# Performance work log

Hardware: AMD Instinct MI355X
Metric: run time of the kernel (lower is better)

The kernel has to match this reference:

```python
import jax, jax.numpy as jnp
import numpy as np

K = 20            # neighbors
C = 21            # num_classes
P = 16            # patch_size
NROWS = 14        # img_size // patch_size
H = NROWS * P     # 224
TEMP = 1.0        # temperature


def setup_inputs() -> dict:
    key = jax.random.key(0)
    k1, k2, k3 = jax.random.split(key, 3)
    test_feature = jax.random.normal(k1, (8, 196, 384), dtype=jnp.float32)
    train_features = jax.random.normal(k2, (384, 50000), dtype=jnp.float32)
    train_labels = jax.random.randint(k3, (256, 50000), 0, C, dtype=jnp.int32)
    return {"test_feature": test_feature, "train_features": train_features,
            "train_labels": train_labels}


def reference(test_feature, train_features, train_labels):
    bs = test_feature.shape[0]
    # similarity: [bs, num_patches, N_train]
    sim = jnp.einsum('bpd,dn->bpn', test_feature, train_features)
    sim_k, idx = jax.lax.top_k(sim, K)              # [bs, 196, K]
    # gather neighbor patch labels: train_labels [P^2, N] -> [bs, 196, K, P^2]
    nb = train_labels.T[idx]
    # make_grid with nrow=NROWS, padding=0: assemble patches into [bs, K, H, H]
    nb = nb.reshape(bs, NROWS, NROWS, K, P, P)
    nb = nb.transpose(0, 3, 1, 4, 2, 5).reshape(bs, K, H, H)
    nb = nb.transpose(0, 2, 3, 1)                   # [bs, H, H, K]
    # weighted majority vote: nearest-upsample similarities 14x14 -> 224x224
    w = sim_k.reshape(bs, NROWS, NROWS, K)
    w = jnp.repeat(jnp.repeat(w, P, axis=1), P, axis=2)   # [bs, H, H, K]
    w = jax.nn.softmax(w / TEMP, axis=-1)
    # one-hot vote expressed as scatter-add over classes (same math, no
    # [bs,H,H,K,C] materialization)
    rows = jnp.arange(bs * H * H)
    vote = jnp.zeros((bs * H * H, C), dtype=w.dtype)
    vote = vote.at[rows[:, None], nb.reshape(bs * H * H, K)].add(
        w.reshape(bs * H * H, K))
    vote = vote.reshape(bs, H, H, C)
    pred = jnp.argmax(vote, axis=-1)                # [bs, H, H] int
    return pred
```

## Files before the change

kernel.cpp:

```cpp
#include <hip/hip_runtime.h>
#include <float.h>

#define N_TRAIN 50000
#define NPAD    50176
#define NBLKS   392
#define MPAD    1664
#define DDIM    384
#define M_ROWS  1568
#define KNN     20
#define K2      24
#define SELMAX  64
#define NCLS    21
#define CAPBUF  768
#define NENT    1568

typedef __attribute__((ext_vector_type(8)))  short bf16x8;
typedef __attribute__((ext_vector_type(16))) float f32x16;

#define GLOAD_LDS16(gp, lp) \
  __builtin_amdgcn_global_load_lds((const __attribute__((address_space(1))) void*)(gp), \
                                   (__attribute__((address_space(3))) void*)(lp), 16, 0, 0)

static __device__ __forceinline__ unsigned short f2bf(float f) {
  unsigned int u = __float_as_uint(f);
  unsigned int r = (u + 0x7fffu + ((u >> 16) & 1u)) >> 16;
  return (unsigned short)r;
}
static __device__ __forceinline__ float bf2f(unsigned short h) {
  return __uint_as_float(((unsigned int)h) << 16);
}
static __device__ __forceinline__ unsigned int flip32(unsigned int u) {
  return (u & 0x80000000u) ? ~u : (u | 0x80000000u);
}

#define CSW(x, y) { unsigned int _hi = max(x, y); unsigned int _lo = min(x, y); x = _hi; y = _lo; }

__global__ __launch_bounds__(256) void transpose_labels(const int* __restrict__ labels,
                                                        unsigned char* __restrict__ labT) {
  __shared__ int tile[64][65];
  const int t  = threadIdx.x;
  const int c0 = blockIdx.x * 64;
  const int r0 = blockIdx.y * 64;
#pragma unroll
  for (int i = 0; i < 16; ++i) {
    int idx = i * 256 + t;
    int r = idx >> 6, c = idx & 63;
    int cc = c0 + c;
    tile[r][c] = (cc < N_TRAIN) ? labels[(size_t)(r0 + r) * N_TRAIN + cc] : 0;
  }
  __syncthreads();
#pragma unroll
  for (int i = 0; i < 16; ++i) {
    int idx = i * 256 + t;
    int c = idx >> 6, r = idx & 63;
    int cc = c0 + c;
    if (cc < N_TRAIN) labT[(size_t)cc * 256 + r0 + r] = (unsigned char)tile[r][c];
  }
}

__global__ __launch_bounds__(256) void conv_Apack(const float* __restrict__ test,
                                                  unsigned short* __restrict__ Apack) {
  int o = blockIdx.x * 256 + threadIdx.x;
  if (o >= (MPAD / 32) * 24 * 512) return;
  int j = o & 7;
  int l = (o >> 3) & 63;
  int rest = o >> 9;
  int ks = rest % 24, mt = rest / 24;
  int row = mt * 32 + (l & 31);
  int k = ks * 16 + (l >> 5) * 8 + j;
  Apack[o] = (row < M_ROWS) ? f2bf(test[(size_t)row * DDIM + k]) : (unsigned short)0;
}

__global__ __launch_bounds__(256) void trans_train_fused(const float* __restrict__ train,
                                                         unsigned short* __restrict__ Bpack,
                                                         float* __restrict__ trainT) {
  __shared__ float tile[64][65];
  const int t  = threadIdx.x;
  const int c0 = blockIdx.x * 64;
  const int r0 = blockIdx.y * 64;
#pragma unroll
  for (int i = 0; i < 16; ++i) {
    int idx = i * 256 + t;
    int r = idx >> 6, c = idx & 63;
    int cc = c0 + c;
    tile[r][c] = (cc < N_TRAIN) ? train[(size_t)(r0 + r) * N_TRAIN + cc] : 0.f;
  }
  __syncthreads();
#pragma unroll
  for (int it = 0; it < 2; ++it) {
    int u = it * 256 + t;
    int c = u & 63, koctL = u >> 6;
    int col = c0 + c;
    int koct = (r0 >> 3) + koctL;
    int ks = koct >> 1, half = koct & 1;
    int nt = col >> 5, l = (c & 31) + half * 32;
    size_t base = ((size_t)(nt * 24 + ks) * 64 + l) * 8;
    ushort4 h0, h1;
    h0.x = f2bf(tile[koctL * 8 + 0][c]); h0.y = f2bf(tile[koctL * 8 + 1][c]);
    h0.z = f2bf(tile[koctL * 8 + 2][c]); h0.w = f2bf(tile[koctL * 8 + 3][c]);
    h1.x = f2bf(tile[koctL * 8 + 4][c]); h1.y = f2bf(tile[koctL * 8 + 5][c]);
    h1.z = f2bf(tile[koctL * 8 + 6][c]); h1.w = f2bf(tile[koctL * 8 + 7][c]);
    *(ushort4*)&Bpack[base]     = h0;
    *(ushort4*)&Bpack[base + 4] = h1;
  }
#pragma unroll
  for (int i = 0; i < 16; ++i) {
    int idx = i * 256 + t;
    int c = idx >> 6, r = idx & 63;
    int cc = c0 + c;
    if (cc < N_TRAIN) trainT[(size_t)cc * DDIM + r0 + r] = tile[r][c];
  }
}

__global__ __launch_bounds__(512, 4) void mfma_gemm(const unsigned short* __restrict__ Apack,
                                                    const unsigned short* __restrict__ Bpack,
                                                    unsigned int* __restrict__ toplist) {
  __shared__ unsigned short Al[24576];
  __shared__ uint4 bounce[64 * 4];
  const int t = threadIdx.x;

  const int flat = blockIdx.x;
  const int xcd = flat & 7, jj = flat >> 3;
  const int wg = (xcd < 2 ? xcd * 160 : 320 + (xcd - 2) * 159) + jj;
  const int mblk = wg % 26, ngrp = wg / 26;
  const int m0 = mblk * 64;

  const int wid = t >> 6, lane = t & 63;
  const int wr = wid >> 2, wc = wid & 3;
  const int l31 = lane & 31, lh = lane >> 5;

  const unsigned short* Asrc = Apack + (size_t)(mblk * 2) * 24 * 512;
#pragma unroll
  for (int j = 0; j < 6; ++j)
    GLOAD_LDS16(Asrc + (size_t)j * 4096 + wid * 512 + lane * 8,
                &Al[j * 4096 + wid * 512]);
  __syncthreads();

#pragma unroll 1
  for (int s = 0; s < 2; ++s) {
    const int colbase = ngrp * 1024 + s * 512;
    const unsigned short* Bb = Bpack + (size_t)((colbase >> 5) + wc * 4) * 24 * 512;

    f32x16 acc[4];
#pragma unroll
    for (int n = 0; n < 4; ++n)
#pragma unroll
      for (int q = 0; q < 16; ++q) acc[n][q] = 0.f;

#pragma unroll 4
    for (int ks = 0; ks < 24; ++ks) {
      bf16x8 a = *(const bf16x8*)&Al[((wr * 24 + ks) * 64 + lane) * 8];
      bf16x8 b[4];
#pragma unroll
      for (int n = 0; n < 4; ++n)
        b[n] = *(const bf16x8*)&Bb[((size_t)(n * 24 + ks) * 64 + lane) * 8];
#pragma unroll
      for (int n = 0; n < 4; ++n)
        acc[n] = __builtin_amdgcn_mfma_f32_32x32x16_bf16(a, b[n], acc[n], 0, 0, 0);
    }

#pragma unroll
    for (int reg = 0; reg < 16; ++reg) {
      const int rowl = (reg & 3) + 8 * (reg >> 2) + 4 * lh;
      unsigned int v0, v1, v2, v3;
      {
        unsigned int e[4];
#pragma unroll
        for (int n = 0; n < 4; ++n) {
          int col = colbase + wc * 128 + n * 32 + l31;
          unsigned int k16 = flip32(__float_as_uint(acc[n][reg])) >> 16;
          e[n] = (col < N_TRAIN) ? ((k16 << 16) | (0xFFFFu - (unsigned int)col)) : 0u;
        }
        CSW(e[0], e[1]); CSW(e[2], e[3]); CSW(e[0], e[2]); CSW(e[1], e[3]); CSW(e[1], e[2]);
        v0 = e[0]; v1 = e[1]; v2 = e[2]; v3 = e[3];
      }
#pragma unroll
      for (int st = 1; st <= 16; st <<= 1) {
        unsigned int p0 = (unsigned int)__shfl_xor((int)v0, st);
        unsigned int p1 = (unsigned int)__shfl_xor((int)v1, st);
        unsigned int p2 = (unsigned int)__shfl_xor((int)v2, st);
        unsigned int p3 = (unsigned int)__shfl_xor((int)v3, st);
        unsigned int t0 = max(v0, p3), t1 = max(v1, p2);
        unsigned int t2 = max(v2, p1), t3 = max(v3, p0);
        CSW(t0, t2); CSW(t1, t3); CSW(t0, t1); CSW(t2, t3);
        v0 = t0; v1 = t1; v2 = t2; v3 = t3;
      }
      if (l31 == 0) {
        uint4 w; w.x = v0; w.y = v1; w.z = v2; w.w = v3;
        bounce[(wr * 32 + rowl) * 4 + wc] = w;
      }
    }
    __syncthreads();

    if (t < 256) {
      int row = t >> 2, e = t & 3;
      int grow = m0 + row;
      if (grow < M_ROWS) {
        uint4 w = bounce[row * 4 + e];
        int blk = (colbase >> 7) + e;
        *(uint4*)&toplist[(size_t)grow * NENT + blk * 4] = w;
      }
    }
    __syncthreads();
  }
}

__global__ __launch_bounds__(256) void tail_fused(const unsigned int* __restrict__ toplist,
                                                  const float* __restrict__ test,
                                                  const float* __restrict__ trainT,
                                                  const unsigned char* __restrict__ labT,
                                                  int* __restrict__ out) {
  const int t = threadIdx.x, m = blockIdx.x;
  __shared__ unsigned int ent[NENT];
  __shared__ unsigned int smax[256];
  __shared__ unsigned int sbuf[CAPBUF];
  __shared__ unsigned int scnt, sTauA, sE24, ccnt2;
  __shared__ unsigned char flg[NBLKS];
  __shared__ short flist[64];
  __shared__ int fcnt, sC2;
  __shared__ unsigned int cbuf[128];
  __shared__ int    selC[SELMAX];
  __shared__ double rvs[SELMAX];
  __shared__ double sv2[SELMAX];
  __shared__ int    si2[SELMAX];
  __shared__ double earr[KNN];
  __shared__ double wv[KNN];
  __shared__ int    wi[KNN];

  if (t == 0) { scnt = 0u; fcnt = 0; ccnt2 = 0u; sC2 = 0; }
  for (int i = t; i < NENT; i += 256) ent[i] = toplist[(size_t)m * NENT + i];
  __syncthreads();

  unsigned int mx = 0u;
  for (int i = t; i < NENT; i += 256) mx = max(mx, ent[i]);
  smax[t] = mx;
  __syncthreads();
  {
    int rnk = 0;
    for (int j = 0; j < 256; ++j)
      rnk += (smax[j] > mx || (smax[j] == mx && j < t)) ? 1 : 0;
    if (rnk == K2 - 1) sTauA = mx;
  }
  __syncthreads();
  const unsigned int tauA = sTauA;

  for (int i = t; i < NENT; i += 256) {
    unsigned int e = ent[i];
    if (e >= tauA) { unsigned int p = atomicAdd(&scnt, 1u); if (p < CAPBUF) sbuf[p] = e; }
  }
  __syncthreads();
  const int C = (int)min(scnt, (unsigned int)CAPBUF);
  for (int s = t; s < C; s += 256) {
    unsigned int e = sbuf[s];
    int rk = 0;
    for (int j = 0; j < C; ++j) rk += (sbuf[j] > e) ? 1 : 0;
    if (rk == K2 - 1) sE24 = e;
  }
  __syncthreads();
  const unsigned int k24 = sE24 >> 16;

  for (int i = t; i < NBLKS; i += 256) {
    bool fl = (ent[i * 4 + 3] >> 16) >= k24;
    flg[i] = fl ? 1 : 0;
    if (fl) { int p = atomicAdd(&fcnt, 1); if (p < 64) flist[p] = (short)i; }
  }
  __syncthreads();

  for (int i = t; i < NENT; i += 256) {
    unsigned int e = ent[i];
    if ((e >> 16) >= k24) {
      int col = 0xFFFF - (int)(e & 0xFFFFu);
      if (!flg[col >> 7]) { unsigned int p = atomicAdd(&ccnt2, 1u); if (p < 128) cbuf[p] = e; }
    }
  }
  __syncthreads();

  const int FC = min(fcnt, 64);
  for (int q = 0; q < FC; ++q) {
    const int fb = flist[q];
    const int col = fb * 128 + t;
    if (t < 128 && col < N_TRAIN) {
      const float* Tc = trainT + (size_t)col * DDIM;
      const float* Tr = test + (size_t)m * DDIM;
      float s0 = 0.f;
      for (int k = 0; k < DDIM; ++k)
        s0 = fmaf(bf2f(f2bf(Tr[k])), bf2f(f2bf(Tc[k])), s0);
      unsigned int key = flip32(__float_as_uint(s0)) >> 16;
      if (key + 1u >= k24) {
        unsigned int e = (key << 16) | (0xFFFFu - (unsigned int)col);
        unsigned int p = atomicAdd(&ccnt2, 1u);
        if (p < 128) cbuf[p] = e;
      }
    }
  }
  __syncthreads();
  const int CC = (int)min(ccnt2, 128u);

  for (int s = t; s < CC; s += 256) {
    unsigned int e = cbuf[s];
    int rk = 0;
    for (int j = 0; j < CC; ++j) rk += (cbuf[j] > e) ? 1 : 0;
    if (rk < SELMAX) {
      selC[rk] = 0xFFFF - (int)(e & 0xFFFFu);
      atomicMax(&sC2, rk + 1);
    }
  }
  __syncthreads();
  const int C2 = sC2 < SELMAX ? sC2 : SELMAX;

  const int wid = t >> 6, lane = t & 63;
  float tr[DDIM / 64];
#pragma unroll
  for (int dd = 0; dd < DDIM / 64; ++dd)
    tr[dd] = test[(size_t)m * DDIM + dd * 64 + lane];
#pragma unroll 1
  for (int c = wid; c < C2; c += 4) {
    const float* Tc = trainT + (size_t)selC[c] * DDIM;
    double s = 0.0;
#pragma unroll
    for (int dd = 0; dd < DDIM / 64; ++dd)
      s += (double)tr[dd] * (double)Tc[dd * 64 + lane];
#pragma unroll
    for (int off = 32; off > 0; off >>= 1) s += __shfl_xor(s, off);
    if (lane == 0) rvs[c] = s;
  }
  __syncthreads();

  if (t < C2) {
    double v = rvs[t]; int id = selC[t];
    int r = 0;
    for (int n = 0; n < C2; ++n)
      r += (rvs[n] > v || (rvs[n] == v && selC[n] < id)) ? 1 : 0;
    sv2[r] = v; si2[r] = id;
  }
  __syncthreads();

  if (t < KNN) earr[t] = exp(sv2[t] - sv2[0]);
  __syncthreads();
  if (t < KNN) {
    double ssum = 0.0;
    for (int k = 0; k < KNN; ++k) ssum += earr[k];
    wv[t] = earr[t] / ssum;
    wi[t] = si2[t];
  }
  __syncthreads();

  unsigned int packed[5];
#pragma unroll
  for (int q = 0; q < 5; ++q) {
    unsigned int p = 0;
#pragma unroll
    for (int j = 0; j < 4; ++j)
      p |= (unsigned int)labT[(size_t)wi[q * 4 + j] * 256 + t] << (8 * j);
    packed[q] = p;
  }
  double best = -1.0; int bc = 0;
#pragma unroll 1
  for (int c = 0; c < NCLS; ++c) {
    double s = 0.0;
#pragma unroll
    for (int k = 0; k < KNN; ++k) {
      unsigned int lab = (packed[k >> 2] >> ((k & 3) * 8)) & 255u;
      s += (lab == (unsigned int)c) ? wv[k] : 0.0;
    }
    if (s > best) { best = s; bc = c; }
  }
  const int b = m / 196, p = m % 196;
  const int py = p / 14, px = p % 14;
  const int i = t >> 4, j = t & 15;
  out[((size_t)b * 224 + py * 16 + i) * 224 + px * 16 + j] = bc;
}

extern "C" void kernel_launch(void* const* d_in, const int* in_sizes, int n_in,
                              void* d_out, int out_size, void* d_ws, size_t ws_size,
                              hipStream_t stream) {
  const float* test  = (const float*)d_in[0];
  const float* train = (const float*)d_in[1];
  const int* labels  = (const int*)d_in[2];
  int* out = (int*)d_out;
  char* ws = (char*)d_ws;

  unsigned char*  labT    = (unsigned char*)ws;
  unsigned short* Apack   = (unsigned short*)(ws + 12800000);
  unsigned short* Bpack   = (unsigned short*)(ws + 14077952);
  float*          trainT  = (float*)(ws + 52613120);
  unsigned int*   toplist = (unsigned int*)(ws + 129413120);

  transpose_labels<<<dim3(782, 4), 256, 0, stream>>>(labels, labT);
  conv_Apack<<<dim3((MPAD / 32) * 24 * 512 / 256), 256, 0, stream>>>(test, Apack);
  trans_train_fused<<<dim3(784, 6), 256, 0, stream>>>(train, Bpack, trainT);
  mfma_gemm<<<dim3(1274), 512, 0, stream>>>(Apack, Bpack, toplist);
  tail_fused<<<dim3(M_ROWS), 256, 0, stream>>>(toplist, test, trainT, labT, out);
}
```

Baseline: 243.6 us.

## Use sampled-prepass threshold to filter GEMM outputs instead of per-block top-4 sorting

Adds a prepass GEMM over the first 3072 training columns and a per-row kernel that picks the 24th-largest key as a threshold. The main GEMM then writes only entries at or above that threshold into fixed 64-slot buckets per row and column group, replacing the shuffle-based sorting network and toplist write. Buckets that overflow are flagged, and the tail recomputes those 1024-column groups exactly. This removes the costly in-register sort but adds two kernels, a memset of about 21 MB, and scattered atomic writes, with the risk that overflow rescans become expensive.

```diff
diff --git a/kernel.cpp b/kernel.cpp
--- a/kernel.cpp
+++ b/kernel.cpp
@@ -2,8 +2,8 @@
 #include <float.h>
 
 #define N_TRAIN 50000
-#define NPAD    50176
-#define NBLKS   392
+#define NBLKG   49
+#define SLOT    64
 #define MPAD    1664
 #define DDIM    384
 #define M_ROWS  1568
@@ -12,7 +12,8 @@
 #define SELMAX  64
 #define NCLS    21
 #define CAPBUF  768
-#define NENT    1568
+#define NENT2   (NBLKG * SLOT)
+#define SAMP    3072
 
 typedef __attribute__((ext_vector_type(8)))  short bf16x8;
 typedef __attribute__((ext_vector_type(16))) float f32x16;
@@ -32,8 +33,6 @@
 static __device__ __forceinline__ unsigned int flip32(unsigned int u) {
   return (u & 0x80000000u) ? ~u : (u | 0x80000000u);
 }
-
-#define CSW(x, y) { unsigned int _hi = max(x, y); unsigned int _lo = min(x, y); x = _hi; y = _lo; }
 
 __global__ __launch_bounds__(256) void transpose_labels(const int* __restrict__ labels,
                                                         unsigned char* __restrict__ labT) {
@@ -112,11 +111,106 @@
   }
 }
 
+__global__ __launch_bounds__(512, 4) void prepass_gemm(const unsigned short* __restrict__ Apack,
+                                                       const unsigned short* __restrict__ Bpack,
+                                                       unsigned short* __restrict__ skey) {
+  __shared__ unsigned short Al[24576];
+  const int t = threadIdx.x;
+  const int mblk = blockIdx.x % 26, scol = blockIdx.x / 26;
+  const int m0 = mblk * 64, colbase = scol * 512;
+  const int wid = t >> 6, lane = t & 63;
+  const int wr = wid >> 2, wc = wid & 3;
+  const int l31 = lane & 31, lh = lane >> 5;
+
+  const unsigned short* Asrc = Apack + (size_t)(mblk * 2) * 24 * 512;
+#pragma unroll
+  for (int j = 0; j < 6; ++j)
+    GLOAD_LDS16(Asrc + (size_t)j * 4096 + wid * 512 + lane * 8,
+                &Al[j * 4096 + wid * 512]);
+  __syncthreads();
+
+  const unsigned short* Bb = Bpack + (size_t)((colbase >> 5) + wc * 4) * 24 * 512;
+  f32x16 acc[4];
+#pragma unroll
+  for (int n = 0; n < 4; ++n)
+#pragma unroll
+    for (int q = 0; q < 16; ++q) acc[n][q] = 0.f;
+
+#pragma unroll 4
+  for (int ks = 0; ks < 24; ++ks) {
+    bf16x8 a = *(const bf16x8*)&Al[((wr * 24 + ks) * 64 + lane) * 8];
+    bf16x8 b[4];
+#pragma unroll
+    for (int n = 0; n < 4; ++n)
+      b[n] = *(const bf16x8*)&Bb[((size_t)(n * 24 + ks) * 64 + lane) * 8];
+#pragma unroll
+    for (int n = 0; n < 4; ++n)
+      acc[n] = __builtin_amdgcn_mfma_f32_32x32x16_bf16(a, b[n], acc[n], 0, 0, 0);
+  }
+
+#pragma unroll
+  for (int reg = 0; reg < 16; ++reg) {
+    const int rowl = (reg & 3) + 8 * (reg >> 2) + 4 * lh;
+    const int row = m0 + wr * 32 + rowl;
+#pragma unroll
+    for (int n = 0; n < 4; ++n) {
+      const int col = colbase + wc * 128 + n * 32 + l31;
+      unsigned int k16 = flip32(__float_as_uint(acc[n][reg])) >> 16;
+      skey[(size_t)row * SAMP + col] = (unsigned short)k16;
+    }
+  }
+}
+
+__global__ __launch_bounds__(256) void tau_kernel(const unsigned short* __restrict__ skey,
+                                                  unsigned short* __restrict__ tau16) {
+  const int m = blockIdx.x, t = threadIdx.x;
+  if (m >= M_ROWS) { if (t == 0) tau16[m] = 0xFFFFu; return; }
+  __shared__ unsigned int smax[256];
+  __shared__ unsigned int sbuf[CAPBUF];
+  __shared__ unsigned int scnt, sTauA, sE24;
+  if (t == 0) { scnt = 0u; sTauA = 0u; sE24 = 0u; }
+  __syncthreads();
+
+  unsigned int mx = 0u;
+  for (int i = t; i < SAMP; i += 256) {
+    unsigned int k = skey[(size_t)m * SAMP + i];
+    unsigned int e = (k << 16) | (0xFFFFu - (unsigned int)i);
+    mx = max(mx, e);
+  }
+  smax[t] = mx;
+  __syncthreads();
+  {
+    int rnk = 0;
+    for (int j = 0; j < 256; ++j) rnk += (smax[j] > mx) ? 1 : 0;
+    if (rnk == K2 - 1) sTauA = mx;
+  }
+  __syncthreads();
+  const unsigned int tauA = sTauA;
+  for (int i = t; i < SAMP; i += 256) {
+    unsigned int k = skey[(size_t)m * SAMP + i];
+    unsigned int e = (k << 16) | (0xFFFFu - (unsigned int)i);
+    if (e >= tauA) { unsigned int p = atomicAdd(&scnt, 1u); if (p < CAPBUF) sbuf[p] = e; }
+  }
+  __syncthreads();
+  const int C = (int)min(scnt, (unsigned int)CAPBUF);
+  for (int s = t; s < C; s += 256) {
+    unsigned int e = sbuf[s];
+    int rk = 0;
+    for (int j = 0; j < C; ++j) rk += (sbuf[j] > e) ? 1 : 0;
+    if (rk == K2 - 1) sE24 = e;
+  }
+  __syncthreads();
+  if (t == 0) tau16[m] = (unsigned short)(sE24 >> 16);
+}
+
 __global__ __launch_bounds__(512, 4) void mfma_gemm(const unsigned short* __restrict__ Apack,
                                                     const unsigned short* __restrict__ Bpack,
-                                                    unsigned int* __restrict__ toplist) {
+                                                    const unsigned short* __restrict__ tau16,
+                                                    unsigned int* __restrict__ surv,
+                                                    unsigned char* __restrict__ ovf) {
   __shared__ unsigned short Al[24576];
-  __shared__ uint4 bounce[64 * 4];
+  __shared__ float Tf[64];
+  __shared__ int cnt[64];
   const int t = threadIdx.x;
 
   const int flat = blockIdx.x;
@@ -129,6 +223,12 @@
   const int wr = wid >> 2, wc = wid & 3;
   const int l31 = lane & 31, lh = lane >> 5;
 
+  if (t < 64) {
+    cnt[t] = 0;
+    unsigned int k = ((unsigned int)tau16[m0 + t]) << 16;
+    unsigned int b = (k & 0x80000000u) ? (k & 0x7fffffffu) : ~k;
+    Tf[t] = __uint_as_float(b);
+  }
   const unsigned short* Asrc = Apack + (size_t)(mblk * 2) * 24 * 512;
 #pragma unroll
   for (int j = 0; j < 6; ++j)
@@ -162,63 +262,45 @@
 #pragma unroll
     for (int reg = 0; reg < 16; ++reg) {
       const int rowl = (reg & 3) + 8 * (reg >> 2) + 4 * lh;
-      unsigned int v0, v1, v2, v3;
-      {
-        unsigned int e[4];
+      const float T = Tf[wr * 32 + rowl];
+      int hit = 0;
+#pragma unroll
+      for (int n = 0; n < 4; ++n) hit |= (acc[n][reg] >= T) ? (1 << n) : 0;
+      if (__any(hit)) {
+        const int row = m0 + wr * 32 + rowl;
 #pragma unroll
         for (int n = 0; n < 4; ++n) {
-          int col = colbase + wc * 128 + n * 32 + l31;
-          unsigned int k16 = flip32(__float_as_uint(acc[n][reg])) >> 16;
-          e[n] = (col < N_TRAIN) ? ((k16 << 16) | (0xFFFFu - (unsigned int)col)) : 0u;
+          if (hit & (1 << n)) {
+            const int col = colbase + wc * 128 + n * 32 + l31;
+            if (col < N_TRAIN) {
+              unsigned int k16 = flip32(__float_as_uint(acc[n][reg])) >> 16;
+              unsigned int e = (k16 << 16) | (0xFFFFu - (unsigned int)col);
+              int slot = atomicAdd(&cnt[wr * 32 + rowl], 1);
+              if (slot < SLOT) surv[((size_t)row * NBLKG + ngrp) * SLOT + slot] = e;
+            }
+          }
         }
-        CSW(e[0], e[1]); CSW(e[2], e[3]); CSW(e[0], e[2]); CSW(e[1], e[3]); CSW(e[1], e[2]);
-        v0 = e[0]; v1 = e[1]; v2 = e[2]; v3 = e[3];
       }
-#pragma unroll
-      for (int st = 1; st <= 16; st <<= 1) {
-        unsigned int p0 = (unsigned int)__shfl_xor((int)v0, st);
-        unsigned int p1 = (unsigned int)__shfl_xor((int)v1, st);
-        unsigned int p2 = (unsigned int)__shfl_xor((int)v2, st);
-        unsigned int p3 = (unsigned int)__shfl_xor((int)v3, st);
-        unsigned int t0 = max(v0, p3), t1 = max(v1, p2);
-        unsigned int t2 = max(v2, p1), t3 = max(v3, p0);
-        CSW(t0, t2); CSW(t1, t3); CSW(t0, t1); CSW(t2, t3);
-        v0 = t0; v1 = t1; v2 = t2; v3 = t3;
-      }
-      if (l31 == 0) {
-        uint4 w; w.x = v0; w.y = v1; w.z = v2; w.w = v3;
-        bounce[(wr * 32 + rowl) * 4 + wc] = w;
-      }
-    }
-    __syncthreads();
-
-    if (t < 256) {
-      int row = t >> 2, e = t & 3;
-      int grow = m0 + row;
-      if (grow < M_ROWS) {
-        uint4 w = bounce[row * 4 + e];
-        int blk = (colbase >> 7) + e;
-        *(uint4*)&toplist[(size_t)grow * NENT + blk * 4] = w;
-      }
-    }
-    __syncthreads();
-  }
-}
-
-__global__ __launch_bounds__(256) void tail_fused(const unsigned int* __restrict__ toplist,
+    }
+  }
+  __syncthreads();
+  if (t < 64 && cnt[t] > SLOT) ovf[(size_t)(m0 + t) * NBLKG + ngrp] = 1;
+}
+
+__global__ __launch_bounds__(256) void tail_fused(const unsigned int* __restrict__ surv,
+                                                  const unsigned char* __restrict__ ovf,
                                                   const float* __restrict__ test,
                                                   const float* __restrict__ trainT,
                                                   const unsigned char* __restrict__ labT,
                                                   int* __restrict__ out) {
   const int t = threadIdx.x, m = blockIdx.x;
-  __shared__ unsigned int ent[NENT];
+  __shared__ unsigned int ent[NENT2];
   __shared__ unsigned int smax[256];
   __shared__ unsigned int sbuf[CAPBUF];
   __shared__ unsigned int scnt, sTauA, sE24, ccnt2;
-  __shared__ unsigned char flg[NBLKS];
   __shared__ short flist[64];
   __shared__ int fcnt, sC2;
-  __shared__ unsigned int cbuf[128];
+  __shared__ unsigned int cbuf[192];
   __shared__ int    selC[SELMAX];
   __shared__ double rvs[SELMAX];
   __shared__ double sv2[SELMAX];
@@ -227,12 +309,14 @@
   __shared__ double wv[KNN];
   __shared__ int    wi[KNN];
 
-  if (t == 0) { scnt = 0u; fcnt = 0; ccnt2 = 0u; sC2 = 0; }
-  for (int i = t; i < NENT; i += 256) ent[i] = toplist[(size_t)m * NENT + i];
+  if (t == 0) { scnt = 0u; fcnt = 0; ccnt2 = 0u; sC2 = 0; sTauA = 0u; sE24 = 0u; }
+  for (int i = t; i < NENT2; i += 256) ent[i] = surv[(size_t)m * NENT2 + i];
+  for (int i = t; i < NBLKG; i += 256)
+    if (ovf[(size_t)m * NBLKG + i]) { int p = atomicAdd(&fcnt, 1); if (p < 64) flist[p] = (short)i; }
   __syncthreads();
 
   unsigned int mx = 0u;
-  for (int i = t; i < NENT; i += 256) mx = max(mx, ent[i]);
+  for (int i = t; i < NENT2; i += 256) mx = max(mx, ent[i]);
   smax[t] = mx;
   __syncthreads();
   {
@@ -244,9 +328,9 @@
   __syncthreads();
   const unsigned int tauA = sTauA;
 
-  for (int i = t; i < NENT; i += 256) {
+  for (int i = t; i < NENT2; i += 256) {
     unsigned int e = ent[i];
-    if (e >= tauA) { unsigned int p = atomicAdd(&scnt, 1u); if (p < CAPBUF) sbuf[p] = e; }
+    if (e != 0u && e >= tauA) { unsigned int p = atomicAdd(&scnt, 1u); if (p < CAPBUF) sbuf[p] = e; }
   }
   __syncthreads();
   const int C = (int)min(scnt, (unsigned int)CAPBUF);
@@ -259,18 +343,11 @@
   __syncthreads();
   const unsigned int k24 = sE24 >> 16;
 
-  for (int i = t; i < NBLKS; i += 256) {
-    bool fl = (ent[i * 4 + 3] >> 16) >= k24;
-    flg[i] = fl ? 1 : 0;
-    if (fl) { int p = atomicAdd(&fcnt, 1); if (p < 64) flist[p] = (short)i; }
-  }
-  __syncthreads();
-
-  for (int i = t; i < NENT; i += 256) {
+  for (int i = t; i < NENT2; i += 256) {
     unsigned int e = ent[i];
-    if ((e >> 16) >= k24) {
-      int col = 0xFFFF - (int)(e & 0xFFFFu);
-      if (!flg[col >> 7]) { unsigned int p = atomicAdd(&ccnt2, 1u); if (p < 128) cbuf[p] = e; }
+    if (e != 0u && (e >> 16) >= k24) {
+      unsigned int p = atomicAdd(&ccnt2, 1u);
+      if (p < 192) cbuf[p] = e;
     }
   }
   __syncthreads();
@@ -278,23 +355,26 @@
   const int FC = min(fcnt, 64);
   for (int q = 0; q < FC; ++q) {
     const int fb = flist[q];
-    const int col = fb * 128 + t;
-    if (t < 128 && col < N_TRAIN) {
-      const float* Tc = trainT + (size_t)col * DDIM;
-      const float* Tr = test + (size_t)m * DDIM;
-      float s0 = 0.f;
-      for (int k = 0; k < DDIM; ++k)
-        s0 = fmaf(bf2f(f2bf(Tr[k])), bf2f(f2bf(Tc[k])), s0);
-      unsigned int key = flip32(__float_as_uint(s0)) >> 16;
-      if (key + 1u >= k24) {
-        unsigned int e = (key << 16) | (0xFFFFu - (unsigned int)col);
-        unsigned int p = atomicAdd(&ccnt2, 1u);
-        if (p < 128) cbuf[p] = e;
+#pragma unroll 1
+    for (int cc = 0; cc < 4; ++cc) {
+      const int col = fb * 1024 + cc * 256 + t;
+      if (col < N_TRAIN) {
+        const float* Tc = trainT + (size_t)col * DDIM;
+        const float* Tr = test + (size_t)m * DDIM;
+        float s0 = 0.f;
+        for (int k = 0; k < DDIM; ++k)
+          s0 = fmaf(bf2f(f2bf(Tr[k])), bf2f(f2bf(Tc[k])), s0);
+        unsigned int key = flip32(__float_as_uint(s0)) >> 16;
+        if (key + 1u >= k24) {
+          unsigned int e = (key << 16) | (0xFFFFu - (unsigned int)col);
+          unsigned int p = atomicAdd(&ccnt2, 1u);
+          if (p < 192) cbuf[p] = e;
+        }
       }
     }
   }
   __syncthreads();
-  const int CC = (int)min(ccnt2, 128u);
+  const int CC = (int)min(ccnt2, 192u);
 
   for (int s = t; s < CC; s += 256) {
     unsigned int e = cbuf[s];
@@ -380,15 +460,21 @@
   int* out = (int*)d_out;
   char* ws = (char*)d_ws;
 
-  unsigned char*  labT    = (unsigned char*)ws;
-  unsigned short* Apack   = (unsigned short*)(ws + 12800000);
-  unsigned short* Bpack   = (unsigned short*)(ws + 14077952);
-  float*          trainT  = (float*)(ws + 52613120);
-  unsigned int*   toplist = (unsigned int*)(ws + 129413120);
-
+  unsigned char*  labT   = (unsigned char*)ws;
+  unsigned short* Apack  = (unsigned short*)(ws + 12800000);
+  unsigned short* Bpack  = (unsigned short*)(ws + 14077952);
+  float*          trainT = (float*)(ws + 52613120);
+  unsigned short* skey   = (unsigned short*)(ws + 129413120);
+  unsigned short* tau16  = (unsigned short*)(ws + 139636736);
+  unsigned int*   surv   = (unsigned int*)(ws + 139640320);
+  unsigned char*  ovf    = (unsigned char*)(ws + 160513536);
+
+  hipMemsetAsync(surv, 0, 20873216 + 81536, stream);
   transpose_labels<<<dim3(782, 4), 256, 0, stream>>>(labels, labT);
   conv_Apack<<<dim3((MPAD / 32) * 24 * 512 / 256), 256, 0, stream>>>(test, Apack);
   trans_train_fused<<<dim3(784, 6), 256, 0, stream>>>(train, Bpack, trainT);
-  mfma_gemm<<<dim3(1274), 512, 0, stream>>>(Apack, Bpack, toplist);
-  tail_fused<<<dim3(M_ROWS), 256, 0, stream>>>(toplist, test, trainT, labT, out);
-}
+  prepass_gemm<<<dim3(156), 512, 0, stream>>>(Apack, Bpack, skey);
+  tau_kernel<<<dim3(MPAD), 256, 0, stream>>>(skey, tau16);
+  mfma_gemm<<<dim3(1274), 512, 0, stream>>>(Apack, Bpack, tau16, surv, ovf);
+  tail_fused<<<dim3(M_ROWS), 256, 0, stream>>>(surv, ovf, test, trainT, labT, out);
+}
```

Measured after the change: 284.8 us. +16.9%, slower.
